# Performance work log

Measured on AMD Instinct MI355X. Metric: run time of the kernel, lower is better.

Reference implementation:

```python
import jax, jax.numpy as jnp
import numpy as np
import math

H = 32          # num_heads
D = 128         # head_dim
HID = 2048      # hidden_size
INNER = H * D   # hidden_inner_size
BLOCK = 256
NUM_LAYERS = 32
LAYER_IDX = 0


def build_slopes(n):
    def p2(m):
        start = 2 ** (-(2 ** (-(math.log2(m) - 3))))
        return [start * (start ** i) for i in range(m)]
    if math.log2(n).is_integer():
        s = p2(n)
    else:
        c = 2 ** math.floor(math.log2(n))
        s = p2(c) + p2(2 * c)[0::2][: n - c]
    s = np.asarray(s, dtype=np.float32)
    s = s * (1.0 - LAYER_IDX / (NUM_LAYERS - 1) + 1e-5)
    return jnp.asarray(s)  # [H]


def lightning_attention(q, k, v, slope, kv0, block):
    # q,k,v: [h,n,d]; slope: [h]; kv0: [h,d,e]
    h, n, d = q.shape
    nb = n // block
    arr = jnp.arange(1, block + 1, dtype=jnp.float32)            # [m]
    s = slope[:, None, None]                                      # [h,1,1]
    q_decay = jnp.exp(-s * arr[None, :, None])                    # [h,m,1]
    k_decay = jnp.exp(-s * (block - arr)[None, :, None])          # [h,m,1]
    idx = arr[:, None] - arr[None, :]                             # [m,m]
    diag_decay = jnp.where(idx >= 0, jnp.exp(-s * idx), 0.0)      # [h,m,m]
    blk_decay = jnp.exp(-slope * block)[:, None, None]            # [h,1,1]

    qb = q.reshape(h, nb, block, d).transpose(1, 0, 2, 3)         # [nb,h,m,d]
    kb = k.reshape(h, nb, block, d).transpose(1, 0, 2, 3)
    vb = v.reshape(h, nb, block, d).transpose(1, 0, 2, 3)

    def step(kv, blk):
        qi, ki, vi = blk
        inter = jnp.einsum('hmd,hde->hme', qi * q_decay, kv)
        qk = jnp.einsum('hmd,hnd->hmn', qi, ki) * diag_decay
        intra = jnp.einsum('hmn,hne->hme', qk, vi)
        kv_new = blk_decay * kv + jnp.einsum('hmd,hme->hde', ki * k_decay, vi)
        return kv_new, inter + intra

    kv_final, out = jax.lax.scan(step, kv0, (qb, kb, vb))
    out = out.transpose(1, 0, 2, 3).reshape(h, n, d)
    return out, kv_final


def rmsnorm(x, w, eps=1e-5):
    xf = x.astype(jnp.float32)
    var = jnp.mean(xf * xf, axis=-1, keepdims=True)
    return (xf * jax.lax.rsqrt(var + eps)).astype(x.dtype) * w


def setup_inputs() -> dict:
    key = jax.random.key(0)
    ks = jax.random.split(key, 4)
    n = 4096
    return {
        'hidden_states': jax.random.normal(ks[0], (n, HID), dtype=jnp.float32),
        'positions': jnp.arange(n, dtype=jnp.int64) if jax.config.jax_enable_x64 else jnp.arange(n, dtype=jnp.int32),
        'kv_cache': jnp.zeros((H, D, D), dtype=jnp.float32),
        'W_qkv': jax.random.normal(ks[1], (HID, 3 * INNER), dtype=jnp.float32) / np.sqrt(HID),
        'W_gate': jax.random.normal(ks[2], (HID, INNER), dtype=jnp.float32) / np.sqrt(HID),
        'W_out': jax.random.normal(ks[3], (INNER, HID), dtype=jnp.float32) / np.sqrt(INNER),
        'norm_weight': jnp.ones((INNER,), dtype=jnp.float32),
    }


def reference(hidden_states, positions, kv_cache, W_qkv, W_gate, W_out, norm_weight):
    n = hidden_states.shape[0]
    slope = build_slopes(H)
    qkv = hidden_states @ W_qkv                                # [n, 3*INNER]
    act = jax.nn.silu(qkv.astype(jnp.float32)).reshape(n, H, 3 * D)
    q, k, v = jnp.split(act, 3, axis=-1)                       # [n,H,D] each
    q = q.transpose(1, 0, 2)                                   # [H,n,D]
    k = k.transpose(1, 0, 2)
    v = v.transpose(1, 0, 2)
    attn, kv_final = lightning_attention(q, k, v, slope, kv_cache.astype(jnp.float32), BLOCK)
    hidden = attn.transpose(1, 0, 2).reshape(n, INNER)          # n (h d)
    hidden = rmsnorm(hidden, norm_weight)
    gate = hidden_states @ W_gate
    hidden = jax.nn.sigmoid(gate) * hidden
    out = hidden @ W_out                                        # [n, HID]
    return out
```

## Files before the change

kernel.cpp:

```cpp
#include <hip/hip_runtime.h>
#include <hip/hip_bf16.h>
#include <cstdint>
#include <cstddef>

#define SEQ    4096
#define HEADS  32
#define HD     128
#define HIDDEN 2048
#define NINNER 4096
#define BLK    256
#define NB     16

typedef __attribute__((ext_vector_type(8)))  __bf16 bf16x8;
typedef __attribute__((ext_vector_type(4)))  __bf16 bf16x4;
typedef __attribute__((ext_vector_type(4)))  float  f32x4;

#define MFMA16(a,b,c) __builtin_amdgcn_mfma_f32_16x16x32_bf16((a),(b),(c),0,0,0)

typedef __attribute__((address_space(1))) const unsigned int gu32;
typedef __attribute__((address_space(3))) unsigned int lu32;

__device__ __forceinline__ void gld16(void* lds, const void* g){
    __builtin_amdgcn_global_load_lds((gu32*)g, (lu32*)lds, 16, 0, 0);
}

__device__ __forceinline__ float slope_for_head(int h){
    return exp2f(-0.25f*(float)(h+1)) * 1.00001f;
}

__device__ __forceinline__ void tcast_block(const float* __restrict__ W, __bf16* __restrict__ Wt,
                                            int K, int N, int bx, int by, __bf16 (*t)[72], int tid){
    const int n0 = bx*64, k0 = by*64;
    const int r = tid >> 4, c4 = tid & 15;
    #pragma unroll
    for (int i = 0; i < 4; i++){
        int k = r + i*16;
        float4 v = *(const float4*)(W + (size_t)(k0 + k)*N + n0 + c4*4);
        t[c4*4+0][k] = (__bf16)v.x;
        t[c4*4+1][k] = (__bf16)v.y;
        t[c4*4+2][k] = (__bf16)v.z;
        t[c4*4+3][k] = (__bf16)v.w;
    }
    __syncthreads();
    #pragma unroll
    for (int j = 0; j < 2; j++){
        int idx = tid + j*256;
        int n = idx >> 3, c8 = idx & 7;
        bf16x8 val = *(const bf16x8*)&t[n][c8*8];
        *(bf16x8*)(Wt + (size_t)(n0 + n)*K + k0 + c8*8) = val;
    }
}

__global__ __launch_bounds__(256)
void prep_all(const float* __restrict__ hs, __bf16* __restrict__ hsb,
              const float* __restrict__ Wqkv, __bf16* __restrict__ WqkvT,
              const float* __restrict__ Wgate, __bf16* __restrict__ WgateT,
              const float* __restrict__ Wout, __bf16* __restrict__ WoutT)
{
    __shared__ __align__(16) __bf16 t[64][72];
    const int tid = threadIdx.x;
    int id = blockIdx.x;
    if (id < 8192){
        int i = (id*256 + tid)*4;
        float4 v = *(const float4*)(hs + i);
        bf16x4 o;
        o[0] = (__bf16)v.x; o[1] = (__bf16)v.y; o[2] = (__bf16)v.z; o[3] = (__bf16)v.w;
        *(bf16x4*)(hsb + i) = o;
    } else if (id < 14336){
        int j = id - 8192;
        tcast_block(Wqkv, WqkvT, 2048, 12288, j % 192, j / 192, t, tid);
    } else if (id < 16384){
        int j = id - 14336;
        tcast_block(Wgate, WgateT, 2048, 4096, j % 64, j / 64, t, tid);
    } else {
        int j = id - 16384;
        tcast_block(Wout, WoutT, 4096, 2048, j % 32, j / 32, t, tid);
    }
}

template<int EPI>
__global__ __launch_bounds__(256,2)
void gemm_bt(const __bf16* __restrict__ A, const __bf16* __restrict__ Bt,
             float* __restrict__ Cf,
             int M, int N, int K)
{
    __shared__ __align__(16) __bf16 a_lds[128*64];
    __shared__ __align__(16) __bf16 b_lds[128*64];
    const int tid  = threadIdx.x;
    const int lane = tid & 63;
    const int w    = tid >> 6;
    const int lr   = lane & 15;
    const int quad = lane >> 4;
    const int wm = w & 1, wn = w >> 1;

    const int bm = blockIdx.x & 31;
    const int bn = blockIdx.x >> 5;

    f32x4 acc[4][4];
    #pragma unroll
    for (int i = 0; i < 4; i++)
        #pragma unroll
        for (int j = 0; j < 4; j++) acc[i][j] = (f32x4){0.f,0.f,0.f,0.f};

    const int r8 = lane >> 3;
    const int qs = (lane & 7) ^ r8;
    const int sw = lr & 7;
    const __bf16* Abase = A  + (size_t)bm*128*K;
    const __bf16* Bbase = Bt + (size_t)bn*128*K;

    for (int kb = 0; kb < K; kb += 64){
        #pragma unroll
        for (int t = 0; t < 4; t++){
            int ch = t*4 + w;
            gld16(a_lds + ch*512, Abase + (size_t)(ch*8 + r8)*K + kb + qs*8);
            gld16(b_lds + ch*512, Bbase + (size_t)(ch*8 + r8)*K + kb + qs*8);
        }
        __syncthreads();
        #pragma unroll
        for (int kk = 0; kk < 2; kk++){
            bf16x8 af[4];
            #pragma unroll
            for (int mt = 0; mt < 4; mt++)
                af[mt] = *(const bf16x8*)&a_lds[(wm*64 + mt*16 + lr)*64 + (((kk*4+quad) ^ sw)*8)];
            #pragma unroll
            for (int nt = 0; nt < 4; nt++){
                bf16x8 bfv = *(const bf16x8*)&b_lds[(wn*64 + nt*16 + lr)*64 + (((kk*4+quad) ^ sw)*8)];
                #pragma unroll
                for (int mt = 0; mt < 4; mt++)
                    acc[mt][nt] = MFMA16(af[mt], bfv, acc[mt][nt]);
            }
        }
        __syncthreads();
    }

    #pragma unroll
    for (int mt = 0; mt < 4; mt++)
    #pragma unroll
    for (int nt = 0; nt < 4; nt++)
    #pragma unroll
    for (int r = 0; r < 4; r++){
        int row = bm*128 + wm*64 + mt*16 + quad*4 + r;
        int col = bn*128 + wn*64 + nt*16 + lr;
        Cf[(size_t)row*N + col] = acc[mt][nt][r];
    }
}

__global__ __launch_bounds__(512, 2)
void gemm_qkv(const __bf16* __restrict__ A, const __bf16* __restrict__ Bt,
              __bf16* __restrict__ qbuf, __bf16* __restrict__ kbuf,
              __bf16* __restrict__ kT,   __bf16* __restrict__ vT,
              __bf16* __restrict__ sgate)
{
    __shared__ __align__(16) __bf16 lds[2][2][2][8192];

    const int tid  = threadIdx.x;
    const int lane = tid & 63;
    const int w    = tid >> 6;
    const int wm   = w & 1;
    const int wn   = w >> 1;
    const int lr   = lane & 15;
    const int quad = lane >> 4;

    const int id  = blockIdx.x;
    const int wg  = (id & 7)*128 + (id >> 3);
    const int bm  = wg & 15;
    const int bn2 = wg >> 4;

    const int l3   = lane >> 3;
    const int lgs  = (lane & 7) ^ l3;
    const int srow = l3*2 + (lgs >> 2);
    const int sg   = lgs & 3;

    const int ag   = ((((lane & 1) << 2) | quad) ^ ((lr >> 1) & 7)) * 8;
    const int aoff = (wm*64 + (lr >> 1))*64 + ag;
    const int boff = (wn*32 + (lr >> 1))*64 + ag;

    const __bf16* Abase = A  + (size_t)bm*256*2048;
    const __bf16* Bbase = Bt + (size_t)bn2*256*2048;

    auto stage = [&](int ab, int buf, int kh, const __bf16* Base, int tcol){
        #pragma unroll
        for (int j = 0; j < 2; j++){
            const int ch = j*8 + w;
            gld16(&lds[ab][buf][kh][ch*512],
                  Base + (size_t)(ch*16 + srow)*2048 + tcol + kh*32 + sg*8);
        }
    };

    f32x4 acc[8][4];
    #pragma unroll
    for (int i = 0; i < 8; i++)
        #pragma unroll
        for (int j = 0; j < 4; j++) acc[i][j] = (f32x4){0.f,0.f,0.f,0.f};

    bf16x8 af[8], bf0, bf1;

    stage(0, 0, 0, Abase, 0);
    stage(1, 0, 0, Bbase, 0);
    stage(0, 0, 1, Abase, 0);
    stage(1, 0, 1, Bbase, 0);
    asm volatile("s_waitcnt vmcnt(4)" ::: "memory");
    __builtin_amdgcn_s_barrier();

    for (int t = 0; t < 32; t++){
        const int c = t & 1, nbuf = c ^ 1;
        const bool pf = (t + 1 < 32);
        const int tcol = (t + 1)*64;

        #pragma unroll
        for (int mt = 0; mt < 8; mt++)
            af[mt] = *(const bf16x8*)&lds[0][c][0][aoff + mt*512];
        bf0 = *(const bf16x8*)&lds[1][c][0][boff];
        bf1 = *(const bf16x8*)&lds[1][c][0][boff + 512];
        if (pf) stage(0, nbuf, 0, Abase, tcol);
        __builtin_amdgcn_s_barrier();
        asm volatile("s_waitcnt lgkmcnt(0)" ::: "memory");
        __builtin_amdgcn_s_setprio(1);
        #pragma unroll
        for (int mt = 0; mt < 8; mt++){
            acc[mt][0] = MFMA16(af[mt], bf0, acc[mt][0]);
            acc[mt][1] = MFMA16(af[mt], bf1, acc[mt][1]);
        }
        __builtin_amdgcn_s_setprio(0);
        __builtin_amdgcn_s_barrier();

        bf0 = *(const bf16x8*)&lds[1][c][0][boff + 1024];
        bf1 = *(const bf16x8*)&lds[1][c][0][boff + 1536];
        if (pf) stage(1, nbuf, 0, Bbase, tcol);
        __builtin_amdgcn_s_barrier();
        asm volatile("s_waitcnt lgkmcnt(0)" ::: "memory");
        __builtin_amdgcn_s_setprio(1);
        #pragma unroll
        for (int mt = 0; mt < 8; mt++){
            acc[mt][2] = MFMA16(af[mt], bf0, acc[mt][2]);
            acc[mt][3] = MFMA16(af[mt], bf1, acc[mt][3]);
        }
        __builtin_amdgcn_s_setprio(0);
        if (pf) { asm volatile("s_waitcnt vmcnt(4)" ::: "memory"); }
        else    { asm volatile("s_waitcnt vmcnt(0)" ::: "memory"); }
        __builtin_amdgcn_s_barrier();

        #pragma unroll
        for (int mt = 0; mt < 8; mt++)
            af[mt] = *(const bf16x8*)&lds[0][c][1][aoff + mt*512];
        bf0 = *(const bf16x8*)&lds[1][c][1][boff];
        bf1 = *(const bf16x8*)&lds[1][c][1][boff + 512];
        if (pf) stage(0, nbuf, 1, Abase, tcol);
        __builtin_amdgcn_s_barrier();
        asm volatile("s_waitcnt lgkmcnt(0)" ::: "memory");
        __builtin_amdgcn_s_setprio(1);
        #pragma unroll
        for (int mt = 0; mt < 8; mt++){
            acc[mt][0] = MFMA16(af[mt], bf0, acc[mt][0]);
            acc[mt][1] = MFMA16(af[mt], bf1, acc[mt][1]);
        }
        __builtin_amdgcn_s_setprio(0);
        __builtin_amdgcn_s_barrier();

        bf0 = *(const bf16x8*)&lds[1][c][1][boff + 1024];
        bf1 = *(const bf16x8*)&lds[1][c][1][boff + 1536];
        if (pf) stage(1, nbuf, 1, Bbase, tcol);
        __builtin_amdgcn_s_barrier();
        asm volatile("s_waitcnt lgkmcnt(0)" ::: "memory");
        __builtin_amdgcn_s_setprio(1);
        #pragma unroll
        for (int mt = 0; mt < 8; mt++){
            acc[mt][2] = MFMA16(af[mt], bf0, acc[mt][2]);
            acc[mt][3] = MFMA16(af[mt], bf1, acc[mt][3]);
        }
        __builtin_amdgcn_s_setprio(0);
        asm volatile("s_waitcnt vmcnt(4)" ::: "memory");
        __builtin_amdgcn_s_barrier();
    }

    const int bn_old = bn2*2 + (wn >> 1);
    const int dbase  = (wn & 1)*64;
    if (bn_old < 96){
        const int h = bn_old/3, which = bn_old - h*3;
        const float s = slope_for_head(h);
        if (which == 0){
            #pragma unroll
            for (int mt = 0; mt < 8; mt++){
                const int pos0 = bm*256 + wm*128 + mt*16 + quad*4;
                #pragma unroll
                for (int nt = 0; nt < 4; nt++){
                    const int d = dbase + nt*16 + lr;
                    #pragma unroll
                    for (int r = 0; r < 4; r++){
                        float x = acc[mt][nt][r];
                        qbuf[((size_t)h*SEQ + pos0 + r)*HD + d] = (__bf16)(x / (1.f + __expf(-x)));
                    }
                }
            }
        } else if (which == 1){
            const float es1 = __expf(s);
            #pragma unroll
            for (int mt = 0; mt < 8; mt++){
                const int pos0 = bm*256 + wm*128 + mt*16 + quad*4;
                const float dec0 = __expf(-s*(float)(255 - (pos0 & 255)));
                #pragma unroll
                for (int nt = 0; nt < 4; nt++){
                    const int d = dbase + nt*16 + lr;
                    float dec = dec0;
                    bf16x4 pk;
                    #pragma unroll
                    for (int r = 0; r < 4; r++){
                        float x = acc[mt][nt][r];
                        float sv = x / (1.f + __expf(-x));
                        kbuf[((size_t)h*SEQ + pos0 + r)*HD + d] = (__bf16)sv;
                        pk[r] = (__bf16)(sv*dec);
                        dec *= es1;
                    }
                    *(bf16x4*)(kT + ((size_t)h*HD + d)*SEQ + pos0) = pk;
                }
            }
        } else {
            #pragma unroll
            for (int mt = 0; mt < 8; mt++){
                const int pos0 = bm*256 + wm*128 + mt*16 + quad*4;
                #pragma unroll
                for (int nt = 0; nt < 4; nt++){
                    const int d = dbase + nt*16 + lr;
                    bf16x4 pv;
                    #pragma unroll
                    for (int r = 0; r < 4; r++){
                        float x = acc[mt][nt][r];
                        pv[r] = (__bf16)(x / (1.f + __expf(-x)));
                    }
                    *(bf16x4*)(vT + ((size_t)h*HD + d)*SEQ + pos0) = pv;
                }
            }
        }
    } else {
        const int col0 = (bn_old - 96)*128 + dbase;
        #pragma unroll
        for (int mt = 0; mt < 8; mt++){
            const int pos0 = bm*256 + wm*128 + mt*16 + quad*4;
            #pragma unroll
            for (int nt = 0; nt < 4; nt++){
                const int col = col0 + nt*16 + lr;
                #pragma unroll
                for (int r = 0; r < 4; r++){
                    float x = acc[mt][nt][r];
                    sgate[(size_t)(pos0 + r)*NINNER + col] = (__bf16)(1.f/(1.f + __expf(-x)));
                }
            }
        }
    }
}

__global__ __launch_bounds__(256,2)
void pass_a(const __bf16* __restrict__ vT, const __bf16* __restrict__ kT,
            float* __restrict__ kvbT)
{
    __shared__ __align__(16) __bf16 a_lds[128*64];
    __shared__ __align__(16) __bf16 b_lds[128*64];
    const int b = blockIdx.x, h = blockIdx.y;
    const int tid = threadIdx.x, lane = tid & 63, w = tid >> 6;
    const int lr = lane & 15, quad = lane >> 4;
    const int wm = w & 1, wn = w >> 1;

    f32x4 acc[4][4];
    #pragma unroll
    for (int i = 0; i < 4; i++)
        #pragma unroll
        for (int j = 0; j < 4; j++) acc[i][j] = (f32x4){0.f,0.f,0.f,0.f};

    const int r8 = lane >> 3;
    const int qs = (lane & 7) ^ r8;
    const int sw = lr & 7;
    const __bf16* Abase = vT + (size_t)h*HD*SEQ + (size_t)b*BLK;
    const __bf16* Bbase = kT + (size_t)h*HD*SEQ + (size_t)b*BLK;

    for (int kb = 0; kb < BLK; kb += 64){
        #pragma unroll
        for (int t = 0; t < 4; t++){
            int ch = t*4 + w;
            gld16(a_lds + ch*512, Abase + (size_t)(ch*8 + r8)*SEQ + kb + qs*8);
            gld16(b_lds + ch*512, Bbase + (size_t)(ch*8 + r8)*SEQ + kb + qs*8);
        }
        __syncthreads();
        #pragma unroll
        for (int kk = 0; kk < 2; kk++){
            bf16x8 af[4];
            #pragma unroll
            for (int mt = 0; mt < 4; mt++)
                af[mt] = *(const bf16x8*)&a_lds[(wm*64 + mt*16 + lr)*64 + (((kk*4+quad) ^ sw)*8)];
            #pragma unroll
            for (int nt = 0; nt < 4; nt++){
                bf16x8 bfv = *(const bf16x8*)&b_lds[(wn*64 + nt*16 + lr)*64 + (((kk*4+quad) ^ sw)*8)];
                #pragma unroll
                for (int mt = 0; mt < 4; mt++)
                    acc[mt][nt] = MFMA16(af[mt], bfv, acc[mt][nt]);
            }
        }
        __syncthreads();
    }
    float* outp = kvbT + (size_t)(h*NB + b)*HD*HD;
    #pragma unroll
    for (int mt = 0; mt < 4; mt++)
    #pragma unroll
    for (int nt = 0; nt < 4; nt++)
    #pragma unroll
    for (int r = 0; r < 4; r++){
        int row = wm*64 + mt*16 + quad*4 + r;
        int col = wn*64 + nt*16 + lr;
        outp[(size_t)row*HD + col] = acc[mt][nt][r];
    }
}

__global__ __launch_bounds__(256)
void scan_kv(const float* __restrict__ kvbT, const float* __restrict__ kv0,
             __bf16* __restrict__ kvsT)
{
    const int chunk = blockIdx.x;
    const int h = blockIdx.y;
    const int t = threadIdx.x;
    const float s = slope_for_head(h);
    const float lam = __expf(-s*(float)BLK);
    const int le0 = chunk*2048;
    float st[8], cur[8], nxt[8];
    #pragma unroll
    for (int j = 0; j < 8; j++){
        int le = le0 + t + 256*j;
        int e = le >> 7, d = le & 127;
        st[j] = kv0[(size_t)h*HD*HD + (size_t)d*HD + e];
    }
    size_t base0 = (size_t)(h*NB)*HD*HD + le0;
    #pragma unroll
    for (int j = 0; j < 8; j++) cur[j] = kvbT[base0 + t + 256*j];
    for (int b = 0; b < NB; b++){
        size_t base = (size_t)(h*NB + b)*HD*HD + le0;
        #pragma unroll
        for (int j = 0; j < 8; j++) kvsT[base + t + 256*j] = (__bf16)st[j];
        if (b < NB-1){
            size_t nb = base + (size_t)HD*HD;
            #pragma unroll
            for (int j = 0; j < 8; j++) nxt[j] = kvbT[nb + t + 256*j];
        }
        #pragma unroll
        for (int j = 0; j < 8; j++){ st[j] = lam*st[j] + cur[j]; cur[j] = nxt[j]; }
    }
}

__global__ __launch_bounds__(256,2)
void pass_c(const __bf16* __restrict__ qbuf, const __bf16* __restrict__ kbuf,
            const __bf16* __restrict__ vT, const __bf16* __restrict__ kvsT,
            float* __restrict__ attn)
{
    __shared__ __align__(16) __bf16 p_lds[4][32*72];
    const int rb = blockIdx.x & 1, b = blockIdx.x >> 1, h = blockIdx.y;
    const float s = slope_for_head(h);
    const int tid = threadIdx.x, lane = tid & 63, w = tid >> 6;
    const int lr = lane & 15, quad = lane >> 4;
    const int R0 = rb*128 + w*32;

    const __bf16* qh  = qbuf + (size_t)h*SEQ*HD + (size_t)b*BLK*HD;
    const __bf16* kh  = kbuf + (size_t)h*SEQ*HD + (size_t)b*BLK*HD;
    const __bf16* vh  = vT   + (size_t)h*HD*SEQ + (size_t)b*BLK;
    const __bf16* kvh = kvsT + (size_t)(h*NB + b)*HD*HD;

    f32x4 acc[2][8];
    #pragma unroll
    for (int i = 0; i < 2; i++)
        #pragma unroll
        for (int j = 0; j < 8; j++) acc[i][j] = (f32x4){0.f,0.f,0.f,0.f};

    bf16x8 qf[4][2];
    #pragma unroll
    for (int ks = 0; ks < 4; ks++)
        #pragma unroll
        for (int mt = 0; mt < 2; mt++)
            qf[ks][mt] = *(const bf16x8*)(qh + (size_t)(R0 + mt*16 + lr)*HD + ks*32 + quad*8);

    float qdec[2];
    #pragma unroll
    for (int mt = 0; mt < 2; mt++)
        qdec[mt] = __expf(-s*(float)(R0 + mt*16 + lr + 1));
    #pragma unroll
    for (int ks = 0; ks < 4; ks++){
        bf16x8 saf[2];
        #pragma unroll
        for (int mt = 0; mt < 2; mt++)
            #pragma unroll
            for (int j = 0; j < 8; j++) saf[mt][j] = (__bf16)((float)qf[ks][mt][j]*qdec[mt]);
        #pragma unroll
        for (int nt = 0; nt < 8; nt++){
            bf16x8 bv = *(const bf16x8*)(kvh + (size_t)(nt*16 + lr)*HD + ks*32 + quad*8);
            #pragma unroll
            for (int mt = 0; mt < 2; mt++) acc[mt][nt] = MFMA16(saf[mt], bv, acc[mt][nt]);
        }
    }

    float colf[4];
    #pragma unroll
    for (int nt = 0; nt < 4; nt++)
        colf[nt] = __expf(-s*(float)(63 - nt*16 - lr));
    const int cmax = (R0 + 31) >> 6;
    for (int c = 0; c <= cmax; c++){
        f32x4 qk[2][4];
        #pragma unroll
        for (int i = 0; i < 2; i++)
            #pragma unroll
            for (int j = 0; j < 4; j++) qk[i][j] = (f32x4){0.f,0.f,0.f,0.f};
        #pragma unroll
        for (int ks = 0; ks < 4; ks++){
            #pragma unroll
            for (int nt = 0; nt < 4; nt++){
                bf16x8 kf = *(const bf16x8*)(kh + (size_t)(c*64 + nt*16 + lr)*HD + ks*32 + quad*8);
                #pragma unroll
                for (int mt = 0; mt < 2; mt++) qk[mt][nt] = MFMA16(qf[ks][mt], kf, qk[mt][nt]);
            }
        }
        float rowf[2][4];
        #pragma unroll
        for (int mt = 0; mt < 2; mt++)
            #pragma unroll
            for (int r = 0; r < 4; r++)
                rowf[mt][r] = __expf(-s*(float)(R0 + mt*16 + quad*4 + r - c*64 - 63));
        #pragma unroll
        for (int mt = 0; mt < 2; mt++)
        #pragma unroll
        for (int nt = 0; nt < 4; nt++)
        #pragma unroll
        for (int r = 0; r < 4; r++){
            int i  = R0 + mt*16 + quad*4 + r;
            int jj = c*64 + nt*16 + lr;
            float dv = (i >= jj) ? rowf[mt][r]*colf[nt] : 0.f;
            p_lds[w][(mt*16 + quad*4 + r)*72 + nt*16 + lr] = (__bf16)(qk[mt][nt][r]*dv);
        }
        #pragma unroll
        for (int ks2 = 0; ks2 < 2; ks2++){
            bf16x8 pf[2];
            #pragma unroll
            for (int mt = 0; mt < 2; mt++)
                pf[mt] = *(const bf16x8*)&p_lds[w][(mt*16 + lr)*72 + ks2*32 + quad*8];
            #pragma unroll
            for (int nt = 0; nt < 8; nt++){
                bf16x8 vf = *(const bf16x8*)(vh + (size_t)(nt*16 + lr)*SEQ + c*64 + ks2*32 + quad*8);
                #pragma unroll
                for (int mt = 0; mt < 2; mt++) acc[mt][nt] = MFMA16(pf[mt], vf, acc[mt][nt]);
            }
        }
    }

    #pragma unroll
    for (int mt = 0; mt < 2; mt++)
    #pragma unroll
    for (int nt = 0; nt < 8; nt++)
    #pragma unroll
    for (int r = 0; r < 4; r++){
        int pos = b*BLK + R0 + mt*16 + quad*4 + r;
        int e = nt*16 + lr;
        attn[(size_t)pos*NINNER + h*HD + e] = acc[mt][nt][r];
    }
}

__global__ __launch_bounds__(256)
void rmsgate(const float* __restrict__ attn, const __bf16* __restrict__ sg,
             const float* __restrict__ nw, __bf16* __restrict__ h2)
{
    const int row = blockIdx.x, tid = threadIdx.x;
    const float* x = attn + (size_t)row*NINNER;
    float4 xs[4];
    float ss = 0.f;
    #pragma unroll
    for (int i = 0; i < 4; i++){
        xs[i] = *(const float4*)(x + (i*256 + tid)*4);
        ss += xs[i].x*xs[i].x + xs[i].y*xs[i].y + xs[i].z*xs[i].z + xs[i].w*xs[i].w;
    }
    #pragma unroll
    for (int o = 32; o > 0; o >>= 1) ss += __shfl_down(ss, o, 64);
    __shared__ float red[4];
    const int lane = tid & 63, w = tid >> 6;
    if (lane == 0) red[w] = ss;
    __syncthreads();
    float tot = red[0] + red[1] + red[2] + red[3];
    float rs = rsqrtf(tot*(1.f/NINNER) + 1e-5f);
    #pragma unroll
    for (int i = 0; i < 4; i++){
        int idx = (i*256 + tid)*4;
        float4 wv = *(const float4*)(nw + idx);
        bf16x4 sv = *(const bf16x4*)(sg + (size_t)row*NINNER + idx);
        bf16x4 o;
        o[0] = (__bf16)((float)sv[0] * xs[i].x*rs*wv.x);
        o[1] = (__bf16)((float)sv[1] * xs[i].y*rs*wv.y);
        o[2] = (__bf16)((float)sv[2] * xs[i].z*rs*wv.z);
        o[3] = (__bf16)((float)sv[3] * xs[i].w*rs*wv.w);
        *(bf16x4*)(h2 + (size_t)row*NINNER + idx) = o;
    }
}

extern "C" void kernel_launch(void* const* d_in, const int* in_sizes, int n_in,
                              void* d_out, int out_size, void* d_ws, size_t ws_size,
                              hipStream_t stream) {
    (void)in_sizes; (void)n_in; (void)out_size; (void)ws_size;
    const float* hs    = (const float*)d_in[0];
    const float* kv0   = (const float*)d_in[2];
    const float* Wqkv  = (const float*)d_in[3];
    const float* Wgate = (const float*)d_in[4];
    const float* Wout  = (const float*)d_in[5];
    const float* nw    = (const float*)d_in[6];
    float* out = (float*)d_out;

    char* ws = (char*)d_ws;
    __bf16* WqkvT  = (__bf16*)(ws);
    __bf16* WgateT = (__bf16*)(ws + 50331648);
    float*  attn   = (float*)(ws);
    __bf16* WoutT  = (__bf16*)(ws + 67108864);
    __bf16* hsb    = (__bf16*)(ws + 83886080);
    __bf16* qkvb   = (__bf16*)(ws + 100663296);
    __bf16* qbuf   = qkvb;
    __bf16* kbuf   = qkvb + (size_t)HEADS*SEQ*HD;
    __bf16* h2     = qkvb;
    __bf16* kT     = (__bf16*)(ws + 201326592);
    __bf16* vT     = (__bf16*)(ws + 234881024);
    float*  kvbT   = (float*) (ws + 268435456);
    __bf16* kvsT   = (__bf16*)(ws + 301989888);
    __bf16* sgate  = (__bf16*)(ws + 318767104);

    prep_all<<<18432, 256, 0, stream>>>(hs, hsb, Wqkv, WqkvT, Wgate, WgateT, Wout, WoutT);

    gemm_qkv<<<1024, 512, 0, stream>>>(hsb, WqkvT, qbuf, kbuf, kT, vT, sgate);

    pass_a<<<dim3(16, 32), 256, 0, stream>>>(vT, kT, kvbT);
    scan_kv<<<dim3(8, 32), 256, 0, stream>>>(kvbT, kv0, kvsT);
    pass_c<<<dim3(NB*2, 32), 256, 0, stream>>>(qbuf, kbuf, vT, kvsT, attn);

    rmsgate<<<4096, 256, 0, stream>>>(attn, sgate, nw, h2);
    gemm_bt<2><<<512, 256, 0, stream>>>(h2, WoutT, out, 4096, 2048, 4096);
}
```

Measured before the change: 715.1 us.

## Deepen QKV GEMM prefetch to 4-stage ring with 32-wide k-steps and new tile order

Replaces the double-buffered 64-wide k-tile pipeline in the QKV GEMM with a 4-slot ring of 32-wide k-slices and three slices in flight. Each B fragment is now loaded once per slice and reused across all 8 M-tiles. The change also adds sched_barriers and remaps the block-to-tile order so groups of blocks share A rows. The aim is to hide global load latency better and cut redundant LDS reads, at the cost of twice as many barrier-separated iterations and more vmcnt bookkeeping.

```diff
diff --git a/kernel.cpp b/kernel.cpp
--- a/kernel.cpp
+++ b/kernel.cpp
@@ -151,7 +151,7 @@
               __bf16* __restrict__ kT,   __bf16* __restrict__ vT,
               __bf16* __restrict__ sgate)
 {
-    __shared__ __align__(16) __bf16 lds[2][2][2][8192];
+    __shared__ __align__(16) __bf16 lds[2][4][8192];
 
     const int tid  = threadIdx.x;
     const int lane = tid & 63;
@@ -162,9 +162,9 @@
     const int quad = lane >> 4;
 
     const int id  = blockIdx.x;
-    const int wg  = (id & 7)*128 + (id >> 3);
-    const int bm  = wg & 15;
-    const int bn2 = wg >> 4;
+    const int u   = id >> 3;
+    const int bm  = u >> 3;
+    const int bn2 = (id & 7)*8 + (u & 7);
 
     const int l3   = lane >> 3;
     const int lgs  = (lane & 7) ^ l3;
@@ -178,12 +178,12 @@
     const __bf16* Abase = A  + (size_t)bm*256*2048;
     const __bf16* Bbase = Bt + (size_t)bn2*256*2048;
 
-    auto stage = [&](int ab, int buf, int kh, const __bf16* Base, int tcol){
+    auto stage = [&](int ab, int buf, const __bf16* Base, int t){
         #pragma unroll
         for (int j = 0; j < 2; j++){
             const int ch = j*8 + w;
-            gld16(&lds[ab][buf][kh][ch*512],
-                  Base + (size_t)(ch*16 + srow)*2048 + tcol + kh*32 + sg*8);
+            gld16(&lds[ab][buf][ch*512],
+                  Base + (size_t)(ch*16 + srow)*2048 + t*32 + sg*8);
         }
     };
 
@@ -193,83 +193,56 @@
         #pragma unroll
         for (int j = 0; j < 4; j++) acc[i][j] = (f32x4){0.f,0.f,0.f,0.f};
 
-    bf16x8 af[8], bf0, bf1;
-
-    stage(0, 0, 0, Abase, 0);
-    stage(1, 0, 0, Bbase, 0);
-    stage(0, 0, 1, Abase, 0);
-    stage(1, 0, 1, Bbase, 0);
-    asm volatile("s_waitcnt vmcnt(4)" ::: "memory");
+    stage(0, 0, Abase, 0); stage(1, 0, Bbase, 0);
+    stage(0, 1, Abase, 1); stage(1, 1, Bbase, 1);
+    stage(0, 2, Abase, 2); stage(1, 2, Bbase, 2);
+    asm volatile("s_waitcnt vmcnt(8)" ::: "memory");
     __builtin_amdgcn_s_barrier();
 
-    for (int t = 0; t < 32; t++){
-        const int c = t & 1, nbuf = c ^ 1;
-        const bool pf = (t + 1 < 32);
-        const int tcol = (t + 1)*64;
-
-        #pragma unroll
-        for (int mt = 0; mt < 8; mt++)
-            af[mt] = *(const bf16x8*)&lds[0][c][0][aoff + mt*512];
-        bf0 = *(const bf16x8*)&lds[1][c][0][boff];
-        bf1 = *(const bf16x8*)&lds[1][c][0][boff + 512];
-        if (pf) stage(0, nbuf, 0, Abase, tcol);
+    for (int t = 0; t < 64; t++){
+        const int c  = t & 3;
+        const int nb = (t + 3) & 3;
+        const bool pf = (t < 61);
+        const int tc = t + 3;
+
+        bf16x8 af0[4], bfv[4];
+        #pragma unroll
+        for (int mt = 0; mt < 4; mt++)
+            af0[mt] = *(const bf16x8*)&lds[0][c][aoff + mt*512];
+        #pragma unroll
+        for (int nt = 0; nt < 4; nt++)
+            bfv[nt] = *(const bf16x8*)&lds[1][c][boff + nt*512];
+        if (pf) stage(0, nb, Abase, tc);
         __builtin_amdgcn_s_barrier();
         asm volatile("s_waitcnt lgkmcnt(0)" ::: "memory");
+        __builtin_amdgcn_sched_barrier(0);
         __builtin_amdgcn_s_setprio(1);
         #pragma unroll
-        for (int mt = 0; mt < 8; mt++){
-            acc[mt][0] = MFMA16(af[mt], bf0, acc[mt][0]);
-            acc[mt][1] = MFMA16(af[mt], bf1, acc[mt][1]);
-        }
+        for (int mt = 0; mt < 4; mt++)
+            #pragma unroll
+            for (int nt = 0; nt < 4; nt++)
+                acc[mt][nt] = MFMA16(af0[mt], bfv[nt], acc[mt][nt]);
         __builtin_amdgcn_s_setprio(0);
         __builtin_amdgcn_s_barrier();
 
-        bf0 = *(const bf16x8*)&lds[1][c][0][boff + 1024];
-        bf1 = *(const bf16x8*)&lds[1][c][0][boff + 1536];
-        if (pf) stage(1, nbuf, 0, Bbase, tcol);
+        bf16x8 af1[4];
+        #pragma unroll
+        for (int mt = 0; mt < 4; mt++)
+            af1[mt] = *(const bf16x8*)&lds[0][c][aoff + (mt+4)*512];
+        if (pf) stage(1, nb, Bbase, tc);
         __builtin_amdgcn_s_barrier();
         asm volatile("s_waitcnt lgkmcnt(0)" ::: "memory");
+        __builtin_amdgcn_sched_barrier(0);
         __builtin_amdgcn_s_setprio(1);
         #pragma unroll
-        for (int mt = 0; mt < 8; mt++){
-            acc[mt][2] = MFMA16(af[mt], bf0, acc[mt][2]);
-            acc[mt][3] = MFMA16(af[mt], bf1, acc[mt][3]);
-        }
+        for (int mt = 0; mt < 4; mt++)
+            #pragma unroll
+            for (int nt = 0; nt < 4; nt++)
+                acc[mt+4][nt] = MFMA16(af1[mt], bfv[nt], acc[mt+4][nt]);
         __builtin_amdgcn_s_setprio(0);
-        if (pf) { asm volatile("s_waitcnt vmcnt(4)" ::: "memory"); }
-        else    { asm volatile("s_waitcnt vmcnt(0)" ::: "memory"); }
-        __builtin_amdgcn_s_barrier();
-
-        #pragma unroll
-        for (int mt = 0; mt < 8; mt++)
-            af[mt] = *(const bf16x8*)&lds[0][c][1][aoff + mt*512];
-        bf0 = *(const bf16x8*)&lds[1][c][1][boff];
-        bf1 = *(const bf16x8*)&lds[1][c][1][boff + 512];
-        if (pf) stage(0, nbuf, 1, Abase, tcol);
-        __builtin_amdgcn_s_barrier();
-        asm volatile("s_waitcnt lgkmcnt(0)" ::: "memory");
-        __builtin_amdgcn_s_setprio(1);
-        #pragma unroll
-        for (int mt = 0; mt < 8; mt++){
-            acc[mt][0] = MFMA16(af[mt], bf0, acc[mt][0]);
-            acc[mt][1] = MFMA16(af[mt], bf1, acc[mt][1]);
-        }
-        __builtin_amdgcn_s_setprio(0);
-        __builtin_amdgcn_s_barrier();
-
-        bf0 = *(const bf16x8*)&lds[1][c][1][boff + 1024];
-        bf1 = *(const bf16x8*)&lds[1][c][1][boff + 1536];
-        if (pf) stage(1, nbuf, 1, Bbase, tcol);
-        __builtin_amdgcn_s_barrier();
-        asm volatile("s_waitcnt lgkmcnt(0)" ::: "memory");
-        __builtin_amdgcn_s_setprio(1);
-        #pragma unroll
-        for (int mt = 0; mt < 8; mt++){
-            acc[mt][2] = MFMA16(af[mt], bf0, acc[mt][2]);
-            acc[mt][3] = MFMA16(af[mt], bf1, acc[mt][3]);
-        }
-        __builtin_amdgcn_s_setprio(0);
-        asm volatile("s_waitcnt vmcnt(4)" ::: "memory");
+        if (t < 61)       { asm volatile("s_waitcnt vmcnt(8)" ::: "memory"); }
+        else if (t == 61) { asm volatile("s_waitcnt vmcnt(4)" ::: "memory"); }
+        else if (t == 62) { asm volatile("s_waitcnt vmcnt(0)" ::: "memory"); }
         __builtin_amdgcn_s_barrier();
     }
 
```

Result: slower. 737.6 us (+3.2%).
